# Kernel tuning notes

Hardware: AMD Instinct MI355X
Metric: run time of the kernel (lower is better)

## Reference

```python
import jax, jax.numpy as jnp
import numpy as np
from jax import lax

B, C, O, K, L, W = 32, 128, 128, 3, 4096, 1
PAD, DIL = 1, 1


def _conv(x, w, b):
    # x: [B,C,H,W], w: [O,C,K,1] -> [B,O,H,W] (zeros padding, stride 1)
    y = lax.conv_general_dilated(x, w, window_strides=(1, 1),
                                 padding=[(PAD, PAD), (0, 0)],
                                 rhs_dilation=(DIL, 1),
                                 dimension_numbers=('NCHW', 'OIHW', 'NCHW'))
    return y + b[None, :, None, None]


def setup_inputs() -> dict:
    key = jax.random.key(0)
    ks = jax.random.split(key, 6)
    x = jax.random.normal(ks[0], (B, C, L, W), dtype=jnp.float32)
    # offset/modulator convs are zero-init in torch; use small random values to
    # exercise the deformable gather path (represents a trained state)
    w_off = jax.random.normal(ks[1], (2 * K, C, K, 1), dtype=jnp.float32) * 0.01
    b_off = jax.random.normal(ks[2], (2 * K,), dtype=jnp.float32) * 0.1
    w_mod = jax.random.normal(ks[3], (K, C, K, 1), dtype=jnp.float32) * 0.01
    b_mod = jax.random.normal(ks[4], (K,), dtype=jnp.float32) * 0.1
    w_reg = jax.random.normal(ks[5], (O, C, K, 1), dtype=jnp.float32) * (1.0 / np.sqrt(C * K))
    return {"x": x, "w_off": w_off, "b_off": b_off,
            "w_mod": w_mod, "b_mod": b_mod, "w_reg": w_reg}


def reference(x, w_off, b_off, w_mod, b_mod, w_reg):
    b, c, h, w = x.shape
    max_offset = max(h, w) / 4.0
    offset = jnp.clip(_conv(x, w_off, b_off), -max_offset, max_offset)  # [B,2K,H,W]
    mask = 2.0 * jax.nn.sigmoid(_conv(x, w_mod, b_mod))                 # [B,K,H,W]

    off = offset.reshape(b, K, 2, h, w)
    off_y, off_x = off[:, :, 0], off[:, :, 1]                           # [B,K,H,W]

    # sampling positions (stride=1, pad_w=0, kw=1)
    base_y = (-PAD + jnp.arange(K, dtype=jnp.float32)[:, None] * DIL
              + jnp.arange(h, dtype=jnp.float32)[None, :])              # [K,H]
    py = base_y[None, :, :, None] + off_y                               # [B,K,H,W]
    px = jnp.arange(w, dtype=jnp.float32)[None, None, None, :] + off_x  # [B,K,H,W]

    y0 = jnp.floor(py); x0 = jnp.floor(px)
    iy0 = y0.astype(jnp.int32); ix0 = x0.astype(jnp.int32)
    wy1 = py - y0; wy0 = 1.0 - wy1
    wx1 = px - x0; wx0 = 1.0 - wx1

    def gather(iy, ix):
        iyc = jnp.clip(iy, 0, h - 1)
        ixc = jnp.clip(ix, 0, w - 1)
        # per-batch gather: xb [C,H,W], idx [K,H,W] -> [C,K,H,W]
        return jax.vmap(lambda xb, yb, xb_i: xb[:, yb, xb_i])(x, iyc, ixc)

    acc = jnp.zeros((b, c, K, h, w), dtype=x.dtype)
    corners = [(iy0, ix0, wy0 * wx0), (iy0, ix0 + 1, wy0 * wx1),
               (iy0 + 1, ix0, wy1 * wx0), (iy0 + 1, ix0 + 1, wy1 * wx1)]
    for iy, ix, wgt in corners:
        valid = ((iy >= 0) & (iy < h) & (ix >= 0) & (ix < w)).astype(x.dtype)
        acc = acc + gather(iy, ix) * (wgt * valid)[:, None]  # [B,C,K,H,W]

    val = acc * mask[:, None]                                 # modulated samples
    out = jnp.einsum('bckhw,ock->bohw', val, w_reg[:, :, :, 0])
    return out
```

## Files before the change

### kernel.cpp

```cpp
#include <hip/hip_runtime.h>
#include <hip/hip_bf16.h>
#include <math.h>


typedef __attribute__((ext_vector_type(8))) short bf16x8;
typedef __attribute__((ext_vector_type(4))) float f32x4;
typedef float f32x2u __attribute__((ext_vector_type(2), aligned(4)));

#define WIN 160
#define WPAD 161

static __device__ inline unsigned short f2bf(float f) {
    __hip_bfloat16 h = __float2bfloat16(f);
    union { __hip_bfloat16 b; unsigned short u; } cv;
    cv.b = h;
    return cv.u;
}

__global__ __launch_bounds__(256) void k_wra(const float* __restrict__ w_reg,
                                             const float* __restrict__ w_off,
                                             const float* __restrict__ w_mod,
                                             unsigned short* __restrict__ WrA,
                                             float* __restrict__ wT) {
    int t = blockIdx.x * 256 + threadIdx.x;
    if (t < 8 * 12 * 64 * 8) {
        int e  = t & 7;
        int l  = (t >> 3) & 63;
        int ms = t >> 9;
        int m  = ms / 12;
        int s  = ms - m * 12;
        int o  = m * 16 + (l & 15);
        int kc = s * 32 + ((l >> 4) & 3) * 8 + e;
        int tap = kc >> 7;
        int c   = kc & 127;
        WrA[t] = f2bf(w_reg[(o * 128 + c) * 3 + tap]);
    } else if (t < 8 * 12 * 64 * 8 + 128 * 27) {
        int u = t - 8 * 12 * 64 * 8;
        int c = u / 27, r = u - c * 27;
        int ch = r / 3, tap = r - ch * 3;
        wT[c * 32 + r] = (ch < 6) ? w_off[(ch * 128 + c) * 3 + tap]
                                  : w_mod[((ch - 6) * 128 + c) * 3 + tap];
    }
}

__global__ __launch_bounds__(256) void k_prep(const float* __restrict__ x,
                                              const float* __restrict__ wT,
                                              const float* __restrict__ b_off,
                                              const float* __restrict__ b_mod,
                                              int* __restrict__ addr2,
                                              float* __restrict__ wae,
                                              float* __restrict__ wbe) {
    __shared__ float red[3 * 64 * 9];
    int t = threadIdx.x;
    int lane = t & 63;
    int wv = t >> 6;
    int b = blockIdx.y;
    int i = blockIdx.x * 64 + lane;

    int c0 = __builtin_amdgcn_readfirstlane(wv) * 32;

    float acc[9];
#pragma unroll
    for (int z = 0; z < 9; ++z) acc[z] = 0.f;

    const float* xr = x + (size_t)b * 524288 + (size_t)c0 * 4096;
    const float* wbase = wT + c0 * 32;
#pragma unroll 2
    for (int c = 0; c < 32; ++c) {
        const float* row = xr + (size_t)c * 4096;
        float xm1v = row[max(i - 1, 0)];
        float x0   = row[i];
        float xp1v = row[min(i + 1, 4095)];
        float xm1 = (i > 0)    ? xm1v : 0.f;
        float xp1 = (i < 4095) ? xp1v : 0.f;
        const float* wrow = wbase + c * 32;
#pragma unroll
        for (int ch = 0; ch < 9; ++ch) {
            acc[ch] += xm1 * wrow[ch * 3 + 0] + x0 * wrow[ch * 3 + 1]
                     + xp1 * wrow[ch * 3 + 2];
        }
    }

    if (wv > 0) {
        float* r = &red[((wv - 1) * 64 + lane) * 9];
#pragma unroll
        for (int z = 0; z < 9; ++z) r[z] = acc[z];
    }
    __syncthreads();
    if (wv != 0) return;

#pragma unroll
    for (int z = 0; z < 9; ++z) {
        acc[z] += red[(0 * 64 + lane) * 9 + z]
                + red[(1 * 64 + lane) * 9 + z]
                + red[(2 * 64 + lane) * 9 + z];
    }

#pragma unroll
    for (int k = 0; k < 3; ++k) {
        float offy = acc[2 * k]     + b_off[2 * k];
        float offx = acc[2 * k + 1] + b_off[2 * k + 1];
        offy = fminf(fmaxf(offy, -1024.f), 1024.f);
        offx = fminf(fmaxf(offx, -1024.f), 1024.f);
        float am = acc[6 + k] + b_mod[k];
        float m  = 2.f / (1.f + expf(-am));

        float py = (float)(i - 1 + k) + offy;
        float y0 = floorf(py);
        int   iy0 = (int)y0;
        float wy1 = py - y0, wy0 = 1.f - wy1;
        float x0f = floorf(offx);
        int   ix0 = (int)x0f;
        float wx1 = offx - x0f, wx0 = 1.f - wx1;

        float sx = (ix0 == 0) ? wx0 : ((ix0 == -1) ? wx1 : 0.f);
        float scal = m * sx;

        float wAv = (iy0 >= 0 && iy0 < 4096)  ? scal * wy0 : 0.f;
        float wBv = (iy0 >= -1 && iy0 < 4095) ? scal * wy1 : 0.f;

        int addr = min(max(iy0, 0), 4094);
        bool eq = (iy0 == addr);
        float wa = eq ? wAv : (iy0 == -1   ? wBv : 0.f);
        float wb = eq ? wBv : (iy0 == 4095 ? wAv : 0.f);

        int j = (b * 3 + k) * 4096 + i;
        addr2[j] = addr;
        wae[j] = wa;
        wbe[j] = wb;
    }
}

__global__ __launch_bounds__(256) void k_fused(const unsigned short* __restrict__ WrA,
                                               const float* __restrict__ x,
                                               const int* __restrict__ addr2,
                                               const float* __restrict__ wae,
                                               const float* __restrict__ wbe,
                                               float* __restrict__ out) {
    __shared__ float win[32 * WPAD];
    int t = threadIdx.x;
    int l = t & 63;
    int w = t >> 6;
    int b  = blockIdx.y;
    int ib = blockIdx.x;
    int q = l >> 4;
    int il = l & 15;
    int f0 = ib * 8 + 2 * w;
    int i0 = f0 * 16 + il;
    int i0t = ib * 128;
    int wsod = i0t - 16;
    if (wsod > 4096 - WIN) wsod = 4096 - WIN;
    if (wsod < 0) wsod = 0;
    const float* xb = x + (size_t)b * 524288;
    const bf16x8* Ag = (const bf16x8*)WrA;

    int   a_[3][2];
    float wa_[3][2], wb_[3][2];
    bool  okw[3][2];
#pragma unroll
    for (int k = 0; k < 3; ++k) {
#pragma unroll
        for (int jj = 0; jj < 2; ++jj) {
            int j = (b * 3 + k) * 4096 + i0 + jj * 16;
            int a = addr2[j];
            a_[k][jj]  = a;
            wa_[k][jj] = wae[j];
            wb_[k][jj] = wbe[j];
            okw[k][jj] = (bool)__all(a >= wsod && a <= wsod + WIN - 2);
        }
    }

    f32x4 acc[8][2];
#pragma unroll
    for (int m = 0; m < 8; ++m) {
        acc[m][0] = (f32x4){0.f, 0.f, 0.f, 0.f};
        acc[m][1] = (f32x4){0.f, 0.f, 0.f, 0.f};
    }

    for (int cc = 0; cc < 4; ++cc) {
        int cb = cc * 32;
        __syncthreads();
#pragma unroll
        for (int it = 0; it < 5; ++it) {
            int idx = it * 256 + t;
            int r  = idx / 40;
            int cp = idx - r * 40;
            float4 v = *(const float4*)(xb + (size_t)(cb + r) * 4096 + wsod + cp * 4);
            float* dst = &win[r * WPAD + cp * 4];
            dst[0] = v.x; dst[1] = v.y; dst[2] = v.z; dst[3] = v.w;
        }
        __syncthreads();

#pragma unroll
        for (int k = 0; k < 3; ++k) {
            int s = k * 4 + cc;
            bf16x8 Bf[2];
#pragma unroll
            for (int jj = 0; jj < 2; ++jj) {
                float v[8];
                float wa = wa_[k][jj], wb = wb_[k][jj];
                if (okw[k][jj]) {
                    int p = a_[k][jj] - wsod;
#pragma unroll
                    for (int e = 0; e < 8; ++e) {
                        const float* base = &win[(q * 8 + e) * WPAD + p];
                        v[e] = wa * base[0] + wb * base[1];
                    }
                } else {
                    int a = a_[k][jj];
#pragma unroll
                    for (int e = 0; e < 8; ++e) {
                        const float* row = xb + (size_t)(cb + q * 8 + e) * 4096;
                        f32x2u p2 = *(const f32x2u*)(row + a);
                        v[e] = wa * p2.x + wb * p2.y;
                    }
                }
                bf16x8 Bv;
#pragma unroll
                for (int e = 0; e < 8; ++e) Bv[e] = (short)f2bf(v[e]);
                Bf[jj] = Bv;
            }
#pragma unroll
            for (int m = 0; m < 8; ++m) {
                bf16x8 A = Ag[(m * 12 + s) * 64 + l];
                acc[m][0] = __builtin_amdgcn_mfma_f32_16x16x32_bf16(A, Bf[0], acc[m][0], 0, 0, 0);
                acc[m][1] = __builtin_amdgcn_mfma_f32_16x16x32_bf16(A, Bf[1], acc[m][1], 0, 0, 0);
            }
        }
    }

    int col = il;
    int r0  = q * 4;
#pragma unroll
    for (int m = 0; m < 8; ++m) {
#pragma unroll
        for (int jj = 0; jj < 2; ++jj) {
            int ig = i0t + (2 * w + jj) * 16 + col;
#pragma unroll
            for (int r = 0; r < 4; ++r) {
                int o = m * 16 + r0 + r;
                out[((size_t)(b * 128 + o)) * 4096 + ig] = acc[m][jj][r];
            }
        }
    }
}

extern "C" void kernel_launch(void* const* d_in, const int* in_sizes, int n_in,
                              void* d_out, int out_size, void* d_ws, size_t ws_size,
                              hipStream_t stream) {
    const float* x     = (const float*)d_in[0];
    const float* w_off = (const float*)d_in[1];
    const float* b_off = (const float*)d_in[2];
    const float* w_mod = (const float*)d_in[3];
    const float* b_mod = (const float*)d_in[4];
    const float* w_reg = (const float*)d_in[5];
    float* out = (float*)d_out;

    char* ws = (char*)d_ws;
    unsigned short* WrA = (unsigned short*)(ws);
    float* wT    = (float*)(ws + 98304);
    int*   addr2 = (int*)  (ws + 131072);
    float* wae   = (float*)(ws + 1703936);
    float* wbe   = (float*)(ws + 3276800);

    k_wra<<<206, 256, 0, stream>>>(w_reg, w_off, w_mod, WrA, wT);
    k_prep<<<dim3(64, 32), 256, 0, stream>>>(x, wT, b_off, b_mod,
                                             addr2, wae, wbe);
    k_fused<<<dim3(32, 32), 256, 0, stream>>>(WrA, x, addr2, wae, wbe, out);
}
```

Baseline: 82.98 us.

## Double-buffer x window in fused kernel; two positions per thread in prep

The fused kernel now double-buffers the shared-memory x window. It issues the global loads for the next 32-channel chunk into registers before running the MFMA work on the current chunk, then writes them to the alternate buffer, so one barrier per chunk is removed and load latency is hidden. The prep kernel now handles two adjacent positions per thread with a float2 load, gets its neighbours through wave shuffles, and writes results as vectors, which halves its grid. The cost is higher register and LDS use, which may lower occupancy.

```diff
diff --git a/kernel.cpp b/kernel.cpp
--- a/kernel.cpp
+++ b/kernel.cpp
@@ -50,84 +50,92 @@
                                               int* __restrict__ addr2,
                                               float* __restrict__ wae,
                                               float* __restrict__ wbe) {
-    __shared__ float red[3 * 64 * 9];
+    __shared__ float red[3 * 64 * 18];
     int t = threadIdx.x;
     int lane = t & 63;
     int wv = t >> 6;
     int b = blockIdx.y;
-    int i = blockIdx.x * 64 + lane;
+    int i = blockIdx.x * 128 + lane * 2;
 
     int c0 = __builtin_amdgcn_readfirstlane(wv) * 32;
 
-    float acc[9];
-#pragma unroll
-    for (int z = 0; z < 9; ++z) acc[z] = 0.f;
+    float acc[18];
+#pragma unroll
+    for (int z = 0; z < 18; ++z) acc[z] = 0.f;
 
     const float* xr = x + (size_t)b * 524288 + (size_t)c0 * 4096;
     const float* wbase = wT + c0 * 32;
 #pragma unroll 2
     for (int c = 0; c < 32; ++c) {
         const float* row = xr + (size_t)c * 4096;
-        float xm1v = row[max(i - 1, 0)];
-        float x0   = row[i];
-        float xp1v = row[min(i + 1, 4095)];
-        float xm1 = (i > 0)    ? xm1v : 0.f;
-        float xp1 = (i < 4095) ? xp1v : 0.f;
+        f32x2u v = *(const f32x2u*)(row + i);
+        float left  = __shfl_up(v.y, 1);
+        float right = __shfl_down(v.x, 1);
+        if (lane == 0)  left  = (i > 0)        ? row[i - 1] : 0.f;
+        if (lane == 63) right = (i + 2 < 4096) ? row[i + 2] : 0.f;
         const float* wrow = wbase + c * 32;
 #pragma unroll
         for (int ch = 0; ch < 9; ++ch) {
-            acc[ch] += xm1 * wrow[ch * 3 + 0] + x0 * wrow[ch * 3 + 1]
-                     + xp1 * wrow[ch * 3 + 2];
+            float w0 = wrow[ch * 3 + 0];
+            float w1 = wrow[ch * 3 + 1];
+            float w2 = wrow[ch * 3 + 2];
+            acc[ch * 2 + 0] += left * w0 + v.x * w1 + v.y  * w2;
+            acc[ch * 2 + 1] += v.x  * w0 + v.y * w1 + right * w2;
         }
     }
 
     if (wv > 0) {
-        float* r = &red[((wv - 1) * 64 + lane) * 9];
-#pragma unroll
-        for (int z = 0; z < 9; ++z) r[z] = acc[z];
+        float* r = &red[((wv - 1) * 64 + lane) * 18];
+#pragma unroll
+        for (int z = 0; z < 18; ++z) r[z] = acc[z];
     }
     __syncthreads();
     if (wv != 0) return;
 
 #pragma unroll
-    for (int z = 0; z < 9; ++z) {
-        acc[z] += red[(0 * 64 + lane) * 9 + z]
-                + red[(1 * 64 + lane) * 9 + z]
-                + red[(2 * 64 + lane) * 9 + z];
+    for (int z = 0; z < 18; ++z) {
+        acc[z] += red[(0 * 64 + lane) * 18 + z]
+                + red[(1 * 64 + lane) * 18 + z]
+                + red[(2 * 64 + lane) * 18 + z];
     }
 
 #pragma unroll
     for (int k = 0; k < 3; ++k) {
-        float offy = acc[2 * k]     + b_off[2 * k];
-        float offx = acc[2 * k + 1] + b_off[2 * k + 1];
-        offy = fminf(fmaxf(offy, -1024.f), 1024.f);
-        offx = fminf(fmaxf(offx, -1024.f), 1024.f);
-        float am = acc[6 + k] + b_mod[k];
-        float m  = 2.f / (1.f + expf(-am));
-
-        float py = (float)(i - 1 + k) + offy;
-        float y0 = floorf(py);
-        int   iy0 = (int)y0;
-        float wy1 = py - y0, wy0 = 1.f - wy1;
-        float x0f = floorf(offx);
-        int   ix0 = (int)x0f;
-        float wx1 = offx - x0f, wx0 = 1.f - wx1;
-
-        float sx = (ix0 == 0) ? wx0 : ((ix0 == -1) ? wx1 : 0.f);
-        float scal = m * sx;
-
-        float wAv = (iy0 >= 0 && iy0 < 4096)  ? scal * wy0 : 0.f;
-        float wBv = (iy0 >= -1 && iy0 < 4095) ? scal * wy1 : 0.f;
-
-        int addr = min(max(iy0, 0), 4094);
-        bool eq = (iy0 == addr);
-        float wa = eq ? wAv : (iy0 == -1   ? wBv : 0.f);
-        float wb = eq ? wBv : (iy0 == 4095 ? wAv : 0.f);
-
+        int   av[2];
+        float wav[2], wbv[2];
+#pragma unroll
+        for (int ii = 0; ii < 2; ++ii) {
+            float offy = acc[(2 * k) * 2 + ii]     + b_off[2 * k];
+            float offx = acc[(2 * k + 1) * 2 + ii] + b_off[2 * k + 1];
+            offy = fminf(fmaxf(offy, -1024.f), 1024.f);
+            offx = fminf(fmaxf(offx, -1024.f), 1024.f);
+            float am = acc[(6 + k) * 2 + ii] + b_mod[k];
+            float m  = 2.f / (1.f + expf(-am));
+
+            float py = (float)(i + ii - 1 + k) + offy;
+            float y0 = floorf(py);
+            int   iy0 = (int)y0;
+            float wy1 = py - y0, wy0 = 1.f - wy1;
+            float x0f = floorf(offx);
+            int   ix0 = (int)x0f;
+            float wx1 = offx - x0f, wx0 = 1.f - wx1;
+
+            float sx = (ix0 == 0) ? wx0 : ((ix0 == -1) ? wx1 : 0.f);
+            float scal = m * sx;
+
+            float wAv = (iy0 >= 0 && iy0 < 4096)  ? scal * wy0 : 0.f;
+            float wBv = (iy0 >= -1 && iy0 < 4095) ? scal * wy1 : 0.f;
+
+            int addr = min(max(iy0, 0), 4094);
+            bool eq = (iy0 == addr);
+            wav[ii] = eq ? wAv : (iy0 == -1   ? wBv : 0.f);
+            wbv[ii] = eq ? wBv : (iy0 == 4095 ? wAv : 0.f);
+            av[ii] = addr;
+        }
         int j = (b * 3 + k) * 4096 + i;
-        addr2[j] = addr;
-        wae[j] = wa;
-        wbe[j] = wb;
+        *(int2*)(addr2 + j)  = make_int2(av[0], av[1]);
+        *(f32x2u*)(wae + j)  = (f32x2u){wav[0], wav[1]};
+        *(f32x2u*)(wbe + j)  = (f32x2u){wbv[0], wbv[1]};
     }
 }
 
@@ -137,7 +145,7 @@
                                                const float* __restrict__ wae,
                                                const float* __restrict__ wbe,
                                                float* __restrict__ out) {
-    __shared__ float win[32 * WPAD];
+    __shared__ float win[2][32 * WPAD];
     int t = threadIdx.x;
     int l = t & 63;
     int w = t >> 6;
@@ -154,6 +162,17 @@
     const float* xb = x + (size_t)b * 524288;
     const bf16x8* Ag = (const bf16x8*)WrA;
 
+    size_t goff_[5];
+    int    loff_[5];
+#pragma unroll
+    for (int it = 0; it < 5; ++it) {
+        int idx = it * 256 + t;
+        int r  = idx / 40;
+        int cp = idx - r * 40;
+        goff_[it] = (size_t)r * 4096 + wsod + cp * 4;
+        loff_[it] = r * WPAD + cp * 4;
+    }
+
     int   a_[3][2];
     float wa_[3][2], wb_[3][2];
     bool  okw[3][2];
@@ -177,20 +196,29 @@
         acc[m][1] = (f32x4){0.f, 0.f, 0.f, 0.f};
     }
 
+    float4 stg[5];
+#pragma unroll
+    for (int it = 0; it < 5; ++it)
+        stg[it] = *(const float4*)(xb + goff_[it]);
+#pragma unroll
+    for (int it = 0; it < 5; ++it) {
+        float* dst = &win[0][loff_[it]];
+        dst[0] = stg[it].x; dst[1] = stg[it].y;
+        dst[2] = stg[it].z; dst[3] = stg[it].w;
+    }
+    __syncthreads();
+
     for (int cc = 0; cc < 4; ++cc) {
+        int pb = cc & 1;
         int cb = cc * 32;
-        __syncthreads();
-#pragma unroll
-        for (int it = 0; it < 5; ++it) {
-            int idx = it * 256 + t;
-            int r  = idx / 40;
-            int cp = idx - r * 40;
-            float4 v = *(const float4*)(xb + (size_t)(cb + r) * 4096 + wsod + cp * 4);
-            float* dst = &win[r * WPAD + cp * 4];
-            dst[0] = v.x; dst[1] = v.y; dst[2] = v.z; dst[3] = v.w;
-        }
-        __syncthreads();
-
+        if (cc < 3) {
+            const float* src = xb + (size_t)(cc + 1) * 131072;
+#pragma unroll
+            for (int it = 0; it < 5; ++it)
+                stg[it] = *(const float4*)(src + goff_[it]);
+        }
+
+        const float* wbuf = win[pb];
 #pragma unroll
         for (int k = 0; k < 3; ++k) {
             int s = k * 4 + cc;
@@ -200,10 +228,10 @@
                 float v[8];
                 float wa = wa_[k][jj], wb = wb_[k][jj];
                 if (okw[k][jj]) {
-                    int p = a_[k][jj] - wsod;
+                    int pos = a_[k][jj] - wsod;
 #pragma unroll
                     for (int e = 0; e < 8; ++e) {
-                        const float* base = &win[(q * 8 + e) * WPAD + p];
+                        const float* base = &wbuf[(q * 8 + e) * WPAD + pos];
                         v[e] = wa * base[0] + wb * base[1];
                     }
                 } else {
@@ -226,6 +254,16 @@
                 acc[m][0] = __builtin_amdgcn_mfma_f32_16x16x32_bf16(A, Bf[0], acc[m][0], 0, 0, 0);
                 acc[m][1] = __builtin_amdgcn_mfma_f32_16x16x32_bf16(A, Bf[1], acc[m][1], 0, 0, 0);
             }
+        }
+
+        if (cc < 3) {
+#pragma unroll
+            for (int it = 0; it < 5; ++it) {
+                float* dst = &win[pb ^ 1][loff_[it]];
+                dst[0] = stg[it].x; dst[1] = stg[it].y;
+                dst[2] = stg[it].z; dst[3] = stg[it].w;
+            }
+            __syncthreads();
         }
     }
 
@@ -264,7 +302,7 @@
     float* wbe   = (float*)(ws + 3276800);
 
     k_wra<<<206, 256, 0, stream>>>(w_reg, w_off, w_mod, WrA, wT);
-    k_prep<<<dim3(64, 32), 256, 0, stream>>>(x, wT, b_off, b_mod,
+    k_prep<<<dim3(32, 32), 256, 0, stream>>>(x, wT, b_off, b_mod,
                                              addr2, wae, wbe);
     k_fused<<<dim3(32, 32), 256, 0, stream>>>(WrA, x, addr2, wae, wbe, out);
 }
```

Result: slower. 90.37 us (+8.9%).
